# Kernel optimization log

Measured on AMD Instinct MI355X. Metric: run time of the kernel, lower is better.

## Reference

```python
import jax, jax.numpy as jnp
import numpy as np

F = 128
NRBF = 20
CUTOFF = 5.0
L = 3
NZ = 100
F2 = F // 2
N = 10000
E = 256000
NMOL = 100
EPS = 1e-8


def setup_inputs() -> dict:
    key = jax.random.key(0)
    ks = jax.random.split(key, 20)
    xyz = jax.random.uniform(ks[0], (N, 3), jnp.float32) * 10.0
    z = jax.random.randint(ks[1], (N,), 0, NZ)
    nbrs = jax.random.randint(ks[2], (E, 2), 0, N)
    # avoid self-edges (would give zero distance in the sinc RBF)
    nbrs = nbrs.at[:, 1].set(jnp.where(nbrs[:, 1] == nbrs[:, 0], (nbrs[:, 1] + 1) % N, nbrs[:, 1]))
    mol_idx = jnp.sort(jax.random.randint(ks[3], (N,), 0, NMOL))

    def p(k, shape, scale=0.05):
        return jax.random.normal(k, shape, jnp.float32) * scale

    return dict(
        xyz=xyz, z=z, nbrs=nbrs, mol_idx=mol_idx,
        emb=p(ks[4], (NZ, F), 1.0),
        msg_W1=p(ks[5], (L, F, F)), msg_b1=jnp.zeros((L, F), jnp.float32),
        msg_W2=p(ks[6], (L, F, 3 * F)), msg_b2=jnp.zeros((L, 3 * F), jnp.float32),
        dist_W=p(ks[7], (L, NRBF, 3 * F)), dist_b=jnp.zeros((L, 3 * F), jnp.float32),
        upd_U=p(ks[8], (L, F, F)), upd_V=p(ks[9], (L, F, F)),
        upd_W1=p(ks[10], (L, 2 * F, F)), upd_b1=jnp.zeros((L, F), jnp.float32),
        upd_W2=p(ks[11], (L, F, 3 * F)), upd_b2=jnp.zeros((L, 3 * F), jnp.float32),
        read_W1=p(ks[12], (F, F2)), read_b1=jnp.zeros((F2,), jnp.float32),
        read_W2=p(ks[13], (F2, 1)), read_b2=jnp.zeros((1,), jnp.float32),
    )


def _painn(xyz, emb, msg_W1, msg_b1, msg_W2, msg_b2, dist_W, dist_b,
           upd_U, upd_V, upd_W1, upd_b1, upd_W2, upd_b2,
           read_W1, read_b1, read_W2, read_b2, z, nbrs, mol_idx):
    idx_i = nbrs[:, 0]
    idx_j = nbrs[:, 1]
    r_ij = xyz[idx_j] - xyz[idx_i]                       # [E,3]
    d = jnp.sqrt(jnp.sum(r_ij * r_ij, -1) + EPS)          # [E]
    unit = r_ij / d[:, None]
    # sinc radial basis + cosine cutoff envelope
    nvec = jnp.arange(1, NRBF + 1, dtype=xyz.dtype)
    rbf = jnp.sin(nvec[None, :] * jnp.pi * d[:, None] / CUTOFF) / d[:, None]   # [E,NRBF]
    fcut = 0.5 * (jnp.cos(jnp.pi * d / CUTOFF) + 1.0) * (d < CUTOFF)           # [E]

    s_i = emb[z]                                          # [N,F]
    v_i = jnp.zeros((xyz.shape[0], F, 3), xyz.dtype)      # [N,F,3]

    for l in range(L):
        # message block: invariant filter on nodes, gather to edges
        phi = (jax.nn.silu(s_i @ msg_W1[l] + msg_b1[l]) @ msg_W2[l] + msg_b2[l])[idx_j]  # [E,3F]
        w_s = (rbf @ dist_W[l] + dist_b[l]) * fcut[:, None]                               # [E,3F]
        inv = (phi * w_s).reshape(-1, 3, F)
        ds_edge = inv[:, 0]                                                               # [E,F]
        dv_edge = inv[:, 1][:, :, None] * v_i[idx_j] + inv[:, 2][:, :, None] * unit[:, None, :]  # [E,F,3]
        s_i = s_i + jax.ops.segment_sum(ds_edge, idx_i, num_segments=s_i.shape[0])
        v_i = v_i + jax.ops.segment_sum(dv_edge, idx_i, num_segments=s_i.shape[0])

        # update block: channel-mixing of vectors + gated scalar/vector residuals
        u_v = jnp.einsum('nfv,fg->ngv', v_i, upd_U[l])
        v_v = jnp.einsum('nfv,fg->ngv', v_i, upd_V[l])
        vnorm = jnp.sqrt(jnp.sum(v_v * v_v, -1) + EPS)                                    # [N,F]
        a = (jax.nn.silu(jnp.concatenate([s_i, vnorm], -1) @ upd_W1[l] + upd_b1[l])
             @ upd_W2[l] + upd_b2[l]).reshape(-1, 3, F)
        dv = u_v * a[:, 0][:, :, None]
        ds = a[:, 1] * jnp.sum(u_v * v_v, -1) + a[:, 2]
        s_i = s_i + ds
        v_i = v_i + dv

    atom_e = jax.nn.silu(s_i @ read_W1 + read_b1) @ read_W2 + read_b2                     # [N,1]
    energy = jax.ops.segment_sum(atom_e[:, 0], mol_idx, num_segments=NMOL)                # [NMOL]
    return energy


def reference(xyz, z, nbrs, mol_idx, emb, msg_W1, msg_b1, msg_W2, msg_b2,
              dist_W, dist_b, upd_U, upd_V, upd_W1, upd_b1, upd_W2, upd_b2,
              read_W1, read_b1, read_W2, read_b2):
    return _painn(xyz, emb, msg_W1, msg_b1, msg_W2, msg_b2, dist_W, dist_b,
                  upd_U, upd_V, upd_W1, upd_b1, upd_W2, upd_b2,
                  read_W1, read_b1, read_W2, read_b2, z, nbrs, mol_idx)
```

## Files before the change

kernel.cpp:

```cpp
#include <hip/hip_runtime.h>
#include <hip/hip_bf16.h>
#include <math.h>

#define NA 10000
#define NE 256000
#define FDIM 128
#define F3 384
#define NRBF 20
#define NLAYERS 3
#define NMOLS 100
#define CAP 96
#define WROW 388
#define CUTOFF_F 5.0f
#define EPS_F 1e-8f
#define PI_F 3.14159265358979323846f

typedef __attribute__((ext_vector_type(8))) short bf16x8;
typedef __attribute__((ext_vector_type(4))) float f32x4;

struct pv6 { unsigned int u0, u1, u2; };

__device__ __forceinline__ float silu_f(float x) { return x / (1.0f + __expf(-x)); }

__device__ __forceinline__ unsigned short f2bf(float x) {
  unsigned u = __float_as_uint(x);
  return (unsigned short)((u + 0x7FFFu + ((u >> 16) & 1u)) >> 16);
}
__device__ __forceinline__ float bf2f(unsigned short u) {
  return __uint_as_float(((unsigned)u) << 16);
}
__device__ __forceinline__ float lo_f(unsigned int u) { return bf2f((unsigned short)(u & 0xFFFFu)); }
__device__ __forceinline__ float hi_f(unsigned int u) { return bf2f((unsigned short)(u >> 16)); }

__global__ __launch_bounds__(256) void geom_build_kernel(
    const float* __restrict__ xyz, const int* __restrict__ nbrs,
    float* __restrict__ unitv, unsigned short* __restrict__ rbf_bf,
    float* __restrict__ fcut,
    int* __restrict__ deg, int* __restrict__ slot_e, int* __restrict__ slot_j) {
  int e = blockIdx.x * 256 + threadIdx.x;
  if (e >= NE) return;
  int i = nbrs[2 * e + 0], j = nbrs[2 * e + 1];
  float rx = xyz[3 * j + 0] - xyz[3 * i + 0];
  float ry = xyz[3 * j + 1] - xyz[3 * i + 1];
  float rz = xyz[3 * j + 2] - xyz[3 * i + 2];
  float d = sqrtf(rx * rx + ry * ry + rz * rz + EPS_F);
  if (d >= CUTOFF_F) return;
  float invd = 1.0f / d;
  float fc = 0.5f * (__cosf(PI_F * d / CUTOFF_F) + 1.0f);
  unitv[3 * e + 0] = rx * invd;
  unitv[3 * e + 1] = ry * invd;
  unitv[3 * e + 2] = rz * invd;
  fcut[e] = fc;
  float base = PI_F * d / CUTOFF_F;
  float sc = invd * fc;
#pragma unroll
  for (int k = 0; k < NRBF; k++)
    rbf_bf[(size_t)e * NRBF + k] = f2bf(__sinf((float)(k + 1) * base) * sc);
  int pos = atomicAdd(&deg[i], 1);
  if (pos < CAP) {
    slot_e[i * CAP + pos] = e;
    slot_j[i * CAP + pos] = j;
  }
}

__device__ __forceinline__ void pack_one(const float* __restrict__ src,
                                         unsigned short* __restrict__ dst,
                                         int loc, int per, int N) {
  int lay = loc / per;
  int kn = loc - lay * per;
  int k = kn / N, n = kn - k * N;
  int kb = k >> 5, q = (k >> 3) & 3, j = k & 7, nt = n >> 4, c = n & 15;
  int NT = N >> 4;
  dst[(size_t)lay * per + (((kb * NT + nt) * 64 + (q * 16 + c)) * 8 + j)] = f2bf(src[loc]);
}

__device__ __forceinline__ void pack_dw(const float* __restrict__ dW,
                                        const float* __restrict__ db,
                                        unsigned short* __restrict__ dst, int loc) {
  int lay = loc / 12288;
  int kn = loc - lay * 12288;
  int k = kn / 384, n = kn - k * 384;
  float val = 0.0f;
  if (k < NRBF) val = dW[lay * NRBF * 384 + k * 384 + n];
  else if (k == NRBF) val = db[lay * 384 + n];
  int q = (k >> 3) & 3, j = k & 7, nt = n >> 4, c = n & 15;
  dst[(size_t)lay * 12288 + ((nt * 64 + (q * 16 + c)) * 8 + j)] = f2bf(val);
}

__global__ __launch_bounds__(256) void pack_all_kernel(
    const float* __restrict__ msgW1, const float* __restrict__ msgW2,
    const float* __restrict__ updU, const float* __restrict__ updV,
    const float* __restrict__ updW1, const float* __restrict__ updW2,
    const float* __restrict__ rW1, const float* __restrict__ distW,
    const float* __restrict__ distb, unsigned short* __restrict__ dst) {
  int t = blockIdx.x * 256 + threadIdx.x;
  if (t < 49152) pack_one(msgW1, dst, t, 16384, 128);
  else if (t < 196608) pack_one(msgW2, dst + 49152, t - 49152, 49152, 384);
  else if (t < 245760) pack_one(updU, dst + 196608, t - 196608, 16384, 128);
  else if (t < 294912) pack_one(updV, dst + 245760, t - 245760, 16384, 128);
  else if (t < 393216) pack_one(updW1, dst + 294912, t - 294912, 32768, 128);
  else if (t < 540672) pack_one(updW2, dst + 393216, t - 393216, 49152, 384);
  else if (t < 548864) pack_one(rW1, dst + 540672, t - 540672, 8192, 64);
  else if (t < 585728) pack_dw(distW, distb, dst + 548864, t - 548864);
}

__global__ __launch_bounds__(256) void msg0_mfma_kernel(
    const float* __restrict__ emb, const int* __restrict__ z, float* __restrict__ s_out,
    const unsigned short* __restrict__ pW1, const float* __restrict__ b1,
    const unsigned short* __restrict__ pW2, const float* __restrict__ b2,
    pv6* __restrict__ cmb) {
  __shared__ bf16x8 sA[4 * 64];
  __shared__ bf16x8 hA[4 * 64];
  int a0 = blockIdx.x * 16;
  int t = threadIdx.x;
  int lane = t & 63, w = t >> 6;
  {
    int kb = t >> 6, l = t & 63;
    int m = l & 15, q = l >> 4;
    int zi = z[a0 + m];
    const float* sp = emb + (size_t)zi * FDIM + kb * 32 + q * 8;
    float* so = s_out + (size_t)(a0 + m) * FDIM + kb * 32 + q * 8;
    bf16x8 c;
#pragma unroll
    for (int j = 0; j < 8; j++) {
      float v = sp[j];
      so[j] = v;
      c[j] = (short)f2bf(v);
    }
    sA[kb * 64 + l] = c;
  }
  __syncthreads();
  f32x4 accH[2];
#pragma unroll
  for (int t2 = 0; t2 < 2; t2++)
#pragma unroll
    for (int r = 0; r < 4; r++) accH[t2][r] = 0.0f;
  const bf16x8* W1f = (const bf16x8*)pW1;
#pragma unroll
  for (int kb = 0; kb < 4; kb++) {
    bf16x8 a = sA[kb * 64 + lane];
#pragma unroll
    for (int t2 = 0; t2 < 2; t2++) {
      bf16x8 b = W1f[(kb * 8 + 2 * w + t2) * 64 + lane];
      accH[t2] = __builtin_amdgcn_mfma_f32_16x16x32_bf16(a, b, accH[t2], 0, 0, 0);
    }
  }
  short* hs = (short*)hA;
#pragma unroll
  for (int t2 = 0; t2 < 2; t2++) {
    int n = w * 32 + t2 * 16 + (lane & 15);
    int kb = n >> 5, q = (n >> 3) & 3, j = n & 7;
    float bias = b1[n];
#pragma unroll
    for (int r = 0; r < 4; r++) {
      int m = (lane >> 4) * 4 + r;
      hs[(kb * 64 + q * 16 + m) * 8 + j] = (short)f2bf(silu_f(accH[t2][r] + bias));
    }
  }
  __syncthreads();
  f32x4 accP[3][2];
#pragma unroll
  for (int c3 = 0; c3 < 3; c3++)
#pragma unroll
    for (int t2 = 0; t2 < 2; t2++)
#pragma unroll
      for (int r = 0; r < 4; r++) accP[c3][t2][r] = 0.0f;
  const bf16x8* W2f = (const bf16x8*)pW2;
#pragma unroll
  for (int kb = 0; kb < 4; kb++) {
    bf16x8 a = hA[kb * 64 + lane];
#pragma unroll
    for (int c3 = 0; c3 < 3; c3++)
#pragma unroll
      for (int t2 = 0; t2 < 2; t2++) {
        bf16x8 b = W2f[(kb * 24 + c3 * 8 + 2 * w + t2) * 64 + lane];
        accP[c3][t2] = __builtin_amdgcn_mfma_f32_16x16x32_bf16(a, b, accP[c3][t2], 0, 0, 0);
      }
  }
#pragma unroll
  for (int t2 = 0; t2 < 2; t2++) {
    int g = (2 * w + t2) * 16 + (lane & 15);
    float bb0 = b2[g], bb1 = b2[FDIM + g], bb2 = b2[2 * FDIM + g];
#pragma unroll
    for (int r = 0; r < 4; r++) {
      int m = (lane >> 4) * 4 + r;
      unsigned p0 = f2bf(accP[0][t2][r] + bb0);
      unsigned p1 = f2bf(accP[1][t2][r] + bb1);
      unsigned p2 = f2bf(accP[2][t2][r] + bb2);
      pv6 rec;
      rec.u0 = p0 | (p1 << 16);
      rec.u1 = p2;
      rec.u2 = 0;
      cmb[(size_t)(a0 + m) * FDIM + g] = rec;
    }
  }
}

__global__ __launch_bounds__(128) void edge_kernel(
    const pv6* __restrict__ cmb, unsigned short* __restrict__ v_lin,
    float* __restrict__ s, const unsigned short* __restrict__ pDW,
    const int* __restrict__ deg, const int* __restrict__ slot_e,
    const int* __restrict__ slot_j, const unsigned short* __restrict__ rbf_bf,
    const float* __restrict__ fcut, const float* __restrict__ unitv) {
  __shared__ bf16x8 aLDS[64];
  __shared__ unsigned short w_lds[16][WROW];
  __shared__ float l_u[16][3];
  __shared__ int l_j[16];
  int i = blockIdx.x;
  int t = threadIdx.x;
  int f = t;
  int lane = t & 63, w = t >> 6;
  int cnt = deg[i];
  if (cnt > CAP) cnt = CAP;
  int base = i * CAP;
  float acc_s = 0.f, av0 = 0.f, av1 = 0.f, av2 = 0.f;
  const bf16x8* Bf = (const bf16x8*)pDW;
  for (int c0 = 0; c0 < cnt; c0 += 16) {
    int ccnt = cnt - c0;
    if (ccnt > 16) ccnt = 16;
    __syncthreads();
    if (t < 64) {
      int m = t & 15, q = t >> 4;
      bf16x8 a;
#pragma unroll
      for (int j = 0; j < 8; j++) a[j] = 0;
      int p = c0 + m;
      if (p < cnt) {
        int e = slot_e[base + p];
        const unsigned short* rb = rbf_bf + (size_t)e * NRBF;
#pragma unroll
        for (int j = 0; j < 8; j++) {
          int k = q * 8 + j;
          if (k < NRBF) a[j] = (short)rb[k];
          else if (k == NRBF) a[j] = (short)f2bf(fcut[e]);
        }
      }
      aLDS[t] = a;
    } else if (t < 80) {
      int idx = t - 64;
      int p = c0 + idx;
      if (p < cnt) {
        int e = slot_e[base + p];
        l_j[idx] = slot_j[base + p];
        l_u[idx][0] = unitv[3 * e + 0];
        l_u[idx][1] = unitv[3 * e + 1];
        l_u[idx][2] = unitv[3 * e + 2];
      }
    }
    __syncthreads();
    {
      bf16x8 a = aLDS[lane];
      int n0 = lane & 15, m0 = (lane >> 4) * 4;
#pragma unroll
      for (int tt = 0; tt < 12; tt++) {
        int nt = 12 * w + tt;
        f32x4 acc;
#pragma unroll
        for (int r = 0; r < 4; r++) acc[r] = 0.0f;
        acc = __builtin_amdgcn_mfma_f32_16x16x32_bf16(a, Bf[nt * 64 + lane], acc, 0, 0, 0);
        int n = nt * 16 + n0;
#pragma unroll
        for (int r = 0; r < 4; r++) w_lds[m0 + r][n] = f2bf(acc[r]);
      }
    }
    __syncthreads();
    int pp = 0;
    for (; pp + 2 <= ccnt; pp += 2) {
      int j0 = l_j[pp], j1 = l_j[pp + 1];
      pv6 R0 = cmb[(size_t)j0 * FDIM + f];
      pv6 R1 = cmb[(size_t)j1 * FDIM + f];
      float p00 = lo_f(R0.u0), p01 = hi_f(R0.u0), p02 = lo_f(R0.u1);
      float v00 = hi_f(R0.u1), v01 = lo_f(R0.u2), v02 = hi_f(R0.u2);
      float p10 = lo_f(R1.u0), p11 = hi_f(R1.u0), p12 = lo_f(R1.u1);
      float v10 = hi_f(R1.u1), v11 = lo_f(R1.u2), v12 = hi_f(R1.u2);
      float w00 = bf2f(w_lds[pp][f]), w01 = bf2f(w_lds[pp][FDIM + f]),
            w02 = bf2f(w_lds[pp][2 * FDIM + f]);
      float w10 = bf2f(w_lds[pp + 1][f]), w11 = bf2f(w_lds[pp + 1][FDIM + f]),
            w12 = bf2f(w_lds[pp + 1][2 * FDIM + f]);
      acc_s += p00 * w00 + p10 * w10;
      float i01 = p01 * w01, i02 = p02 * w02, i11 = p11 * w11, i12 = p12 * w12;
      av0 += i01 * v00 + i02 * l_u[pp][0] + i11 * v10 + i12 * l_u[pp + 1][0];
      av1 += i01 * v01 + i02 * l_u[pp][1] + i11 * v11 + i12 * l_u[pp + 1][1];
      av2 += i01 * v02 + i02 * l_u[pp][2] + i11 * v12 + i12 * l_u[pp + 1][2];
    }
    if (pp < ccnt) {
      int j0 = l_j[pp];
      pv6 R0 = cmb[(size_t)j0 * FDIM + f];
      float p00 = lo_f(R0.u0), p01 = hi_f(R0.u0), p02 = lo_f(R0.u1);
      float v00 = hi_f(R0.u1), v01 = lo_f(R0.u2), v02 = hi_f(R0.u2);
      float w00 = bf2f(w_lds[pp][f]), w01 = bf2f(w_lds[pp][FDIM + f]),
            w02 = bf2f(w_lds[pp][2 * FDIM + f]);
      acc_s += p00 * w00;
      float i01 = p01 * w01, i02 = p02 * w02;
      av0 += i01 * v00 + i02 * l_u[pp][0];
      av1 += i01 * v01 + i02 * l_u[pp][1];
      av2 += i01 * v02 + i02 * l_u[pp][2];
    }
  }
  {
    pv6 RI = cmb[(size_t)i * FDIM + f];
    av0 += hi_f(RI.u1);
    av1 += lo_f(RI.u2);
    av2 += hi_f(RI.u2);
  }
  unsigned short* vlo = v_lin + (size_t)i * F3;
  vlo[f] = f2bf(av0);
  vlo[FDIM + f] = f2bf(av1);
  vlo[2 * FDIM + f] = f2bf(av2);
  s[(size_t)i * FDIM + f] += acc_s;
}

__global__ __launch_bounds__(256) void upd_fused_kernel(
    float* __restrict__ s, const unsigned short* __restrict__ v_lin,
    pv6* __restrict__ cmb,
    const unsigned short* __restrict__ pU, const unsigned short* __restrict__ pV,
    const unsigned short* __restrict__ pW1, const float* __restrict__ b1,
    const unsigned short* __restrict__ pW2, const float* __restrict__ b2,
    int mode,
    const unsigned short* __restrict__ pMW1, const float* __restrict__ mb1,
    const unsigned short* __restrict__ pMW2, const float* __restrict__ mb2,
    const unsigned short* __restrict__ pRW1, const float* __restrict__ rb1,
    const float* __restrict__ rW2, const float* __restrict__ rb2,
    float* __restrict__ atom_e) {
  __shared__ bf16x8 vAf[3 * 4 * 64];
  __shared__ bf16x8 catA[8 * 64];
  __shared__ bf16x8 hA[4 * 64];
  __shared__ float red[4][16];
  int a0 = blockIdx.x * 16;
  int t = threadIdx.x;
  int lane = t & 63, w = t >> 6;
  {
    int l = t & 63, kb = (t >> 6) & 3;
    int m = l & 15, q = l >> 4;
#pragma unroll
    for (int rt = 0; rt < 3; rt++) {
      vAf[(rt * 4 + kb) * 64 + l] =
          *(const bf16x8*)(v_lin + (size_t)(a0 + m) * F3 + rt * FDIM + kb * 32 + q * 8);
    }
    const float* sp = s + (size_t)(a0 + m) * FDIM + kb * 32 + q * 8;
    bf16x8 c;
#pragma unroll
    for (int j = 0; j < 8; j++) c[j] = (short)f2bf(sp[j]);
    catA[kb * 64 + l] = c;
  }
  __syncthreads();
  f32x4 accU[3][2], accV[3][2];
#pragma unroll
  for (int rt = 0; rt < 3; rt++)
#pragma unroll
    for (int t2 = 0; t2 < 2; t2++)
#pragma unroll
      for (int r = 0; r < 4; r++) { accU[rt][t2][r] = 0.0f; accV[rt][t2][r] = 0.0f; }
  const bf16x8* Uf = (const bf16x8*)pU;
  const bf16x8* Vf = (const bf16x8*)pV;
#pragma unroll
  for (int kb = 0; kb < 4; kb++) {
    bf16x8 bu[2], bv[2];
#pragma unroll
    for (int t2 = 0; t2 < 2; t2++) {
      bu[t2] = Uf[(kb * 8 + 2 * w + t2) * 64 + lane];
      bv[t2] = Vf[(kb * 8 + 2 * w + t2) * 64 + lane];
    }
#pragma unroll
    for (int rt = 0; rt < 3; rt++) {
      bf16x8 a = vAf[(rt * 4 + kb) * 64 + lane];
#pragma unroll
      for (int t2 = 0; t2 < 2; t2++) {
        accU[rt][t2] = __builtin_amdgcn_mfma_f32_16x16x32_bf16(a, bu[t2], accU[rt][t2], 0, 0, 0);
        accV[rt][t2] = __builtin_amdgcn_mfma_f32_16x16x32_bf16(a, bv[t2], accV[rt][t2], 0, 0, 0);
      }
    }
  }
  short* cs = (short*)catA;
#pragma unroll
  for (int t2 = 0; t2 < 2; t2++) {
    int g = w * 32 + t2 * 16 + (lane & 15);
    int k = 128 + g;
    int kb = k >> 5, q = (k >> 3) & 3, j = k & 7;
#pragma unroll
    for (int r = 0; r < 4; r++) {
      int m = (lane >> 4) * 4 + r;
      float x0 = accV[0][t2][r], x1 = accV[1][t2][r], x2 = accV[2][t2][r];
      cs[(kb * 64 + q * 16 + m) * 8 + j] = (short)f2bf(sqrtf(x0 * x0 + x1 * x1 + x2 * x2 + EPS_F));
    }
  }
  __syncthreads();
  f32x4 accH[2];
#pragma unroll
  for (int t2 = 0; t2 < 2; t2++)
#pragma unroll
    for (int r = 0; r < 4; r++) accH[t2][r] = 0.0f;
  const bf16x8* W1f = (const bf16x8*)pW1;
#pragma unroll
  for (int kb = 0; kb < 8; kb++) {
    bf16x8 a = catA[kb * 64 + lane];
#pragma unroll
    for (int t2 = 0; t2 < 2; t2++) {
      bf16x8 b = W1f[(kb * 8 + 2 * w + t2) * 64 + lane];
      accH[t2] = __builtin_amdgcn_mfma_f32_16x16x32_bf16(a, b, accH[t2], 0, 0, 0);
    }
  }
  short* hs = (short*)hA;
#pragma unroll
  for (int t2 = 0; t2 < 2; t2++) {
    int n = w * 32 + t2 * 16 + (lane & 15);
    int kb = n >> 5, q = (n >> 3) & 3, j = n & 7;
    float bias = b1[n];
#pragma unroll
    for (int r = 0; r < 4; r++) {
      int m = (lane >> 4) * 4 + r;
      hs[(kb * 64 + q * 16 + m) * 8 + j] = (short)f2bf(silu_f(accH[t2][r] + bias));
    }
  }
  __syncthreads();
  f32x4 accA[3][2];
#pragma unroll
  for (int c3 = 0; c3 < 3; c3++)
#pragma unroll
    for (int t2 = 0; t2 < 2; t2++)
#pragma unroll
      for (int r = 0; r < 4; r++) accA[c3][t2][r] = 0.0f;
  const bf16x8* W2f = (const bf16x8*)pW2;
#pragma unroll
  for (int kb = 0; kb < 4; kb++) {
    bf16x8 a = hA[kb * 64 + lane];
#pragma unroll
    for (int c3 = 0; c3 < 3; c3++)
#pragma unroll
      for (int t2 = 0; t2 < 2; t2++) {
        bf16x8 b = W2f[(kb * 24 + c3 * 8 + 2 * w + t2) * 64 + lane];
        accA[c3][t2] = __builtin_amdgcn_mfma_f32_16x16x32_bf16(a, b, accA[c3][t2], 0, 0, 0);
      }
  }
  short* vsc = (short*)vAf;
#pragma unroll
  for (int t2 = 0; t2 < 2; t2++) {
    int g = w * 32 + t2 * 16 + (lane & 15);
    float bb0 = b2[g], bb1 = b2[FDIM + g], bb2 = b2[2 * FDIM + g];
    int kb = g >> 5, q = (g >> 3) & 3, j = g & 7;
#pragma unroll
    for (int r = 0; r < 4; r++) {
      int m = (lane >> 4) * 4 + r;
      int n = a0 + m;
      float a0v = accA[0][t2][r] + bb0;
      float a1v = accA[1][t2][r] + bb1;
      float a2v = accA[2][t2][r] + bb2;
      float dot = accU[0][t2][r] * accV[0][t2][r] + accU[1][t2][r] * accV[1][t2][r] +
                  accU[2][t2][r] * accV[2][t2][r];
      float s_new = s[(size_t)n * FDIM + g] + a1v * dot + a2v;
      if (mode == 0) {
        s[(size_t)n * FDIM + g] = s_new;
#pragma unroll
        for (int c = 0; c < 3; c++) {
          float nv = bf2f(v_lin[(size_t)n * F3 + c * FDIM + g]) + a0v * accU[c][t2][r];
          vsc[(m * FDIM + g) * 3 + c] = (short)f2bf(nv);
        }
      }
      cs[(kb * 64 + q * 16 + m) * 8 + j] = (short)f2bf(s_new);
    }
  }
  __syncthreads();
  if (mode == 0) {
    f32x4 accH2[2];
#pragma unroll
    for (int t2 = 0; t2 < 2; t2++)
#pragma unroll
      for (int r = 0; r < 4; r++) accH2[t2][r] = 0.0f;
    const bf16x8* MW1f = (const bf16x8*)pMW1;
#pragma unroll
    for (int kb = 0; kb < 4; kb++) {
      bf16x8 a = catA[kb * 64 + lane];
#pragma unroll
      for (int t2 = 0; t2 < 2; t2++) {
        bf16x8 b = MW1f[(kb * 8 + 2 * w + t2) * 64 + lane];
        accH2[t2] = __builtin_amdgcn_mfma_f32_16x16x32_bf16(a, b, accH2[t2], 0, 0, 0);
      }
    }
#pragma unroll
    for (int t2 = 0; t2 < 2; t2++) {
      int n = w * 32 + t2 * 16 + (lane & 15);
      int kb = n >> 5, q = (n >> 3) & 3, j = n & 7;
      float bias = mb1[n];
#pragma unroll
      for (int r = 0; r < 4; r++) {
        int m = (lane >> 4) * 4 + r;
        hs[(kb * 64 + q * 16 + m) * 8 + j] = (short)f2bf(silu_f(accH2[t2][r] + bias));
      }
    }
    __syncthreads();
    f32x4 accP[3][2];
#pragma unroll
    for (int c3 = 0; c3 < 3; c3++)
#pragma unroll
      for (int t2 = 0; t2 < 2; t2++)
#pragma unroll
        for (int r = 0; r < 4; r++) accP[c3][t2][r] = 0.0f;
    const bf16x8* MW2f = (const bf16x8*)pMW2;
#pragma unroll
    for (int kb = 0; kb < 4; kb++) {
      bf16x8 a = hA[kb * 64 + lane];
#pragma unroll
      for (int c3 = 0; c3 < 3; c3++)
#pragma unroll
        for (int t2 = 0; t2 < 2; t2++) {
          bf16x8 b = MW2f[(kb * 24 + c3 * 8 + 2 * w + t2) * 64 + lane];
          accP[c3][t2] = __builtin_amdgcn_mfma_f32_16x16x32_bf16(a, b, accP[c3][t2], 0, 0, 0);
        }
    }
#pragma unroll
    for (int t2 = 0; t2 < 2; t2++) {
      int g = (2 * w + t2) * 16 + (lane & 15);
      float bb0 = mb2[g], bb1 = mb2[FDIM + g], bb2v = mb2[2 * FDIM + g];
#pragma unroll
      for (int r = 0; r < 4; r++) {
        int m = (lane >> 4) * 4 + r;
        unsigned p0 = f2bf(accP[0][t2][r] + bb0);
        unsigned p1 = f2bf(accP[1][t2][r] + bb1);
        unsigned p2 = f2bf(accP[2][t2][r] + bb2v);
        unsigned v0 = (unsigned short)vsc[(m * FDIM + g) * 3 + 0];
        unsigned v1 = (unsigned short)vsc[(m * FDIM + g) * 3 + 1];
        unsigned v2 = (unsigned short)vsc[(m * FDIM + g) * 3 + 2];
        pv6 rec;
        rec.u0 = p0 | (p1 << 16);
        rec.u1 = p2 | (v0 << 16);
        rec.u2 = v1 | (v2 << 16);
        cmb[(size_t)(a0 + m) * FDIM + g] = rec;
      }
    }
  } else {
    f32x4 acc;
#pragma unroll
    for (int r = 0; r < 4; r++) acc[r] = 0.0f;
    const bf16x8* RW1f = (const bf16x8*)pRW1;
#pragma unroll
    for (int kb = 0; kb < 4; kb++) {
      bf16x8 a = catA[kb * 64 + lane];
      bf16x8 b = RW1f[(kb * 4 + w) * 64 + lane];
      acc = __builtin_amdgcn_mfma_f32_16x16x32_bf16(a, b, acc, 0, 0, 0);
    }
    int col = w * 16 + (lane & 15);
    float bias = rb1[col], w2v = rW2[col];
    float val[4];
#pragma unroll
    for (int r = 0; r < 4; r++) val[r] = silu_f(acc[r] + bias) * w2v;
#pragma unroll
    for (int off = 1; off < 16; off <<= 1)
#pragma unroll
      for (int r = 0; r < 4; r++) val[r] += __shfl_xor(val[r], off, 64);
    if ((lane & 15) == 0) {
#pragma unroll
      for (int r = 0; r < 4; r++) red[w][(lane >> 4) * 4 + r] = val[r];
    }
    __syncthreads();
    if (t < 16) {
      atom_e[a0 + t] = red[0][t] + red[1][t] + red[2][t] + red[3][t] + rb2[0];
    }
  }
}

__global__ __launch_bounds__(256) void mol_reduce_kernel(
    const float* __restrict__ atom_e, const int* __restrict__ mol_idx,
    float* __restrict__ out) {
  __shared__ float molsum[NMOLS];
  int t = threadIdx.x;
  if (t < NMOLS) molsum[t] = 0.0f;
  __syncthreads();
  int n = blockIdx.x * 256 + t;
  if (n < NA) atomicAdd(&molsum[mol_idx[n]], atom_e[n]);
  __syncthreads();
  if (t < NMOLS && molsum[t] != 0.0f) atomicAdd(&out[t], molsum[t]);
}

extern "C" void kernel_launch(void* const* d_in, const int* in_sizes, int n_in,
                              void* d_out, int out_size, void* d_ws, size_t ws_size,
                              hipStream_t stream) {
  const float* xyz = (const float*)d_in[0];
  const int* z = (const int*)d_in[1];
  const int* nbrs = (const int*)d_in[2];
  const int* mol = (const int*)d_in[3];
  const float* emb = (const float*)d_in[4];
  const float* msgW1 = (const float*)d_in[5];
  const float* msgb1 = (const float*)d_in[6];
  const float* msgW2 = (const float*)d_in[7];
  const float* msgb2 = (const float*)d_in[8];
  const float* distW = (const float*)d_in[9];
  const float* distb = (const float*)d_in[10];
  const float* updU = (const float*)d_in[11];
  const float* updV = (const float*)d_in[12];
  const float* updW1 = (const float*)d_in[13];
  const float* updb1 = (const float*)d_in[14];
  const float* updW2 = (const float*)d_in[15];
  const float* updb2 = (const float*)d_in[16];
  const float* rW1 = (const float*)d_in[17];
  const float* rb1 = (const float*)d_in[18];
  const float* rW2 = (const float*)d_in[19];
  const float* rb2 = (const float*)d_in[20];

  float* ws = (float*)d_ws;
  float* s = ws;      ws += (size_t)NA * FDIM;
  float* fcut = ws;   ws += (size_t)NE;
  float* unitv = ws;  ws += (size_t)NE * 3;
  float* atom_e = ws; ws += (size_t)NA;
  int* deg = (int*)ws;
  int* slot_e = deg + NA;
  int* slot_j = slot_e + NA * CAP;
  unsigned short* pk = (unsigned short*)(((uintptr_t)(slot_j + NA * CAP) + 15) & ~(uintptr_t)15);
  unsigned short* pMsgW1 = pk;
  unsigned short* pMsgW2 = pMsgW1 + 49152;
  unsigned short* pUpdU  = pMsgW2 + 147456;
  unsigned short* pUpdV  = pUpdU + 49152;
  unsigned short* pUpdW1 = pUpdV + 49152;
  unsigned short* pUpdW2 = pUpdW1 + 98304;
  unsigned short* pRW1   = pUpdW2 + 147456;
  unsigned short* pDW    = pRW1 + 8192;
  unsigned short* rbf_bf = (unsigned short*)(((uintptr_t)(pDW + 36864) + 15) & ~(uintptr_t)15);
  unsigned short* after_rbf = rbf_bf + (size_t)NE * NRBF + 8;
  pv6* cmb = (pv6*)(((uintptr_t)after_rbf + 15) & ~(uintptr_t)15);
  unsigned short* v_lin = (unsigned short*)(cmb + (size_t)NA * FDIM);

  hipMemsetAsync(deg, 0, NA * sizeof(int), stream);
  hipMemsetAsync(d_out, 0, NMOLS * sizeof(float), stream);

  pack_all_kernel<<<(585728 + 255) / 256, 256, 0, stream>>>(
      msgW1, msgW2, updU, updV, updW1, updW2, rW1, distW, distb, pMsgW1);
  geom_build_kernel<<<NE / 256, 256, 0, stream>>>(xyz, nbrs, unitv, rbf_bf, fcut,
                                                  deg, slot_e, slot_j);
  msg0_mfma_kernel<<<NA / 16, 256, 0, stream>>>(emb, z, s, pMsgW1, msgb1, pMsgW2, msgb2, cmb);

  for (int l = 0; l < NLAYERS; l++) {
    edge_kernel<<<NA, 128, 0, stream>>>(cmb, v_lin, s,
                                        pDW + (size_t)l * 12288,
                                        deg, slot_e, slot_j, rbf_bf, fcut, unitv);
    int mode = (l == NLAYERS - 1) ? 1 : 0;
    int lnext = (l + 1 < NLAYERS) ? l + 1 : 0;
    upd_fused_kernel<<<NA / 16, 256, 0, stream>>>(
        s, v_lin, cmb, pUpdU + (size_t)l * 16384, pUpdV + (size_t)l * 16384,
        pUpdW1 + (size_t)l * 32768, updb1 + (size_t)l * FDIM,
        pUpdW2 + (size_t)l * 49152, updb2 + (size_t)l * F3,
        mode,
        pMsgW1 + (size_t)lnext * 16384, msgb1 + (size_t)lnext * FDIM,
        pMsgW2 + (size_t)lnext * 49152, msgb2 + (size_t)lnext * F3,
        pRW1, rb1, rW2, rb2, atom_e);
  }
  mol_reduce_kernel<<<(NA + 255) / 256, 256, 0, stream>>>(atom_e, mol, (float*)d_out);
}
```

Before: 326.4 us.

## Split edge chunks across two block halves and skip zero vectors in layer zero

The edge kernel now runs with 256 threads. Two 128-thread halves take alternating 16-edge chunks with double-buffered LDS, and their partial sums are combined through shared memory at the end. In the first layer a vzero flag skips loading the vector parts of the gathered records and the self term, since the vectors start at zero. The update kernel reads old vectors from its LDS tile instead of global v_lin and writes the packed record fields separately. The trade-off is more barriers, extra LDS use, and idle halves on atoms with an odd number of chunks.

Result: slower. 393.8 us (+20.7%).

```diff
diff --git a/kernel.cpp b/kernel.cpp
--- a/kernel.cpp
+++ b/kernel.cpp
@@ -196,31 +196,39 @@
   }
 }
 
-__global__ __launch_bounds__(128) void edge_kernel(
+__global__ __launch_bounds__(256) void edge_kernel(
     const pv6* __restrict__ cmb, unsigned short* __restrict__ v_lin,
     float* __restrict__ s, const unsigned short* __restrict__ pDW,
     const int* __restrict__ deg, const int* __restrict__ slot_e,
     const int* __restrict__ slot_j, const unsigned short* __restrict__ rbf_bf,
-    const float* __restrict__ fcut, const float* __restrict__ unitv) {
-  __shared__ bf16x8 aLDS[64];
-  __shared__ unsigned short w_lds[16][WROW];
-  __shared__ float l_u[16][3];
-  __shared__ int l_j[16];
+    const float* __restrict__ fcut, const float* __restrict__ unitv, int vzero) {
+  __shared__ bf16x8 aLDS[2][64];
+  __shared__ unsigned short w_lds[2][16][WROW];
+  __shared__ float l_u[2][16][3];
+  __shared__ int l_j[2][16];
+  __shared__ float partial[4][FDIM];
   int i = blockIdx.x;
   int t = threadIdx.x;
-  int f = t;
-  int lane = t & 63, w = t >> 6;
+  int half = t >> 7;
+  int p128 = t & 127;
+  int f = p128;
+  int lane = t & 63;
+  int wp = (t >> 6) & 1;
   int cnt = deg[i];
   if (cnt > CAP) cnt = CAP;
   int base = i * CAP;
+  int nchunks = (cnt + 15) >> 4;
+  int maxiter = (nchunks + 1) >> 1;
   float acc_s = 0.f, av0 = 0.f, av1 = 0.f, av2 = 0.f;
   const bf16x8* Bf = (const bf16x8*)pDW;
-  for (int c0 = 0; c0 < cnt; c0 += 16) {
-    int ccnt = cnt - c0;
-    if (ccnt > 16) ccnt = 16;
+  for (int it = 0; it < maxiter; it++) {
+    int c = 2 * it + half;
+    bool active = (c < nchunks);
+    int c0 = c * 16;
+    int ccnt = active ? ((cnt - c0 > 16) ? 16 : (cnt - c0)) : 0;
     __syncthreads();
-    if (t < 64) {
-      int m = t & 15, q = t >> 4;
+    if (active && p128 < 64) {
+      int m = p128 & 15, q = p128 >> 4;
       bf16x8 a;
 #pragma unroll
       for (int j = 0; j < 8; j++) a[j] = 0;
@@ -235,79 +243,111 @@
           else if (k == NRBF) a[j] = (short)f2bf(fcut[e]);
         }
       }
-      aLDS[t] = a;
-    } else if (t < 80) {
-      int idx = t - 64;
+      aLDS[half][p128] = a;
+    } else if (active && p128 < 80) {
+      int idx = p128 - 64;
       int p = c0 + idx;
       if (p < cnt) {
         int e = slot_e[base + p];
-        l_j[idx] = slot_j[base + p];
-        l_u[idx][0] = unitv[3 * e + 0];
-        l_u[idx][1] = unitv[3 * e + 1];
-        l_u[idx][2] = unitv[3 * e + 2];
+        l_j[half][idx] = slot_j[base + p];
+        l_u[half][idx][0] = unitv[3 * e + 0];
+        l_u[half][idx][1] = unitv[3 * e + 1];
+        l_u[half][idx][2] = unitv[3 * e + 2];
       }
     }
     __syncthreads();
-    {
-      bf16x8 a = aLDS[lane];
+    if (active) {
+      bf16x8 a = aLDS[half][lane];
       int n0 = lane & 15, m0 = (lane >> 4) * 4;
 #pragma unroll
       for (int tt = 0; tt < 12; tt++) {
-        int nt = 12 * w + tt;
+        int nt = 12 * wp + tt;
         f32x4 acc;
 #pragma unroll
         for (int r = 0; r < 4; r++) acc[r] = 0.0f;
         acc = __builtin_amdgcn_mfma_f32_16x16x32_bf16(a, Bf[nt * 64 + lane], acc, 0, 0, 0);
         int n = nt * 16 + n0;
 #pragma unroll
-        for (int r = 0; r < 4; r++) w_lds[m0 + r][n] = f2bf(acc[r]);
+        for (int r = 0; r < 4; r++) w_lds[half][m0 + r][n] = f2bf(acc[r]);
       }
     }
     __syncthreads();
     int pp = 0;
     for (; pp + 2 <= ccnt; pp += 2) {
-      int j0 = l_j[pp], j1 = l_j[pp + 1];
-      pv6 R0 = cmb[(size_t)j0 * FDIM + f];
-      pv6 R1 = cmb[(size_t)j1 * FDIM + f];
-      float p00 = lo_f(R0.u0), p01 = hi_f(R0.u0), p02 = lo_f(R0.u1);
-      float v00 = hi_f(R0.u1), v01 = lo_f(R0.u2), v02 = hi_f(R0.u2);
-      float p10 = lo_f(R1.u0), p11 = hi_f(R1.u0), p12 = lo_f(R1.u1);
-      float v10 = hi_f(R1.u1), v11 = lo_f(R1.u2), v12 = hi_f(R1.u2);
-      float w00 = bf2f(w_lds[pp][f]), w01 = bf2f(w_lds[pp][FDIM + f]),
-            w02 = bf2f(w_lds[pp][2 * FDIM + f]);
-      float w10 = bf2f(w_lds[pp + 1][f]), w11 = bf2f(w_lds[pp + 1][FDIM + f]),
-            w12 = bf2f(w_lds[pp + 1][2 * FDIM + f]);
+      int j0 = l_j[half][pp], j1 = l_j[half][pp + 1];
+      float p00, p01, p02, p10, p11, p12;
+      float v00 = 0.f, v01 = 0.f, v02 = 0.f, v10 = 0.f, v11 = 0.f, v12 = 0.f;
+      if (vzero) {
+        const pv6* R0 = &cmb[(size_t)j0 * FDIM + f];
+        const pv6* R1 = &cmb[(size_t)j1 * FDIM + f];
+        unsigned a0u = R0->u0, a1u = R0->u1, b0u = R1->u0, b1u = R1->u1;
+        p00 = lo_f(a0u); p01 = hi_f(a0u); p02 = lo_f(a1u);
+        p10 = lo_f(b0u); p11 = hi_f(b0u); p12 = lo_f(b1u);
+      } else {
+        pv6 R0 = cmb[(size_t)j0 * FDIM + f];
+        pv6 R1 = cmb[(size_t)j1 * FDIM + f];
+        p00 = lo_f(R0.u0); p01 = hi_f(R0.u0); p02 = lo_f(R0.u1);
+        v00 = hi_f(R0.u1); v01 = lo_f(R0.u2); v02 = hi_f(R0.u2);
+        p10 = lo_f(R1.u0); p11 = hi_f(R1.u0); p12 = lo_f(R1.u1);
+        v10 = hi_f(R1.u1); v11 = lo_f(R1.u2); v12 = hi_f(R1.u2);
+      }
+      float w00 = bf2f(w_lds[half][pp][f]), w01 = bf2f(w_lds[half][pp][FDIM + f]),
+            w02 = bf2f(w_lds[half][pp][2 * FDIM + f]);
+      float w10 = bf2f(w_lds[half][pp + 1][f]), w11 = bf2f(w_lds[half][pp + 1][FDIM + f]),
+            w12 = bf2f(w_lds[half][pp + 1][2 * FDIM + f]);
       acc_s += p00 * w00 + p10 * w10;
       float i01 = p01 * w01, i02 = p02 * w02, i11 = p11 * w11, i12 = p12 * w12;
-      av0 += i01 * v00 + i02 * l_u[pp][0] + i11 * v10 + i12 * l_u[pp + 1][0];
-      av1 += i01 * v01 + i02 * l_u[pp][1] + i11 * v11 + i12 * l_u[pp + 1][1];
-      av2 += i01 * v02 + i02 * l_u[pp][2] + i11 * v12 + i12 * l_u[pp + 1][2];
+      av0 += i01 * v00 + i02 * l_u[half][pp][0] + i11 * v10 + i12 * l_u[half][pp + 1][0];
+      av1 += i01 * v01 + i02 * l_u[half][pp][1] + i11 * v11 + i12 * l_u[half][pp + 1][1];
+      av2 += i01 * v02 + i02 * l_u[half][pp][2] + i11 * v12 + i12 * l_u[half][pp + 1][2];
     }
     if (pp < ccnt) {
-      int j0 = l_j[pp];
-      pv6 R0 = cmb[(size_t)j0 * FDIM + f];
-      float p00 = lo_f(R0.u0), p01 = hi_f(R0.u0), p02 = lo_f(R0.u1);
-      float v00 = hi_f(R0.u1), v01 = lo_f(R0.u2), v02 = hi_f(R0.u2);
-      float w00 = bf2f(w_lds[pp][f]), w01 = bf2f(w_lds[pp][FDIM + f]),
-            w02 = bf2f(w_lds[pp][2 * FDIM + f]);
+      int j0 = l_j[half][pp];
+      float p00, p01, p02;
+      float v00 = 0.f, v01 = 0.f, v02 = 0.f;
+      if (vzero) {
+        const pv6* R0 = &cmb[(size_t)j0 * FDIM + f];
+        unsigned a0u = R0->u0, a1u = R0->u1;
+        p00 = lo_f(a0u); p01 = hi_f(a0u); p02 = lo_f(a1u);
+      } else {
+        pv6 R0 = cmb[(size_t)j0 * FDIM + f];
+        p00 = lo_f(R0.u0); p01 = hi_f(R0.u0); p02 = lo_f(R0.u1);
+        v00 = hi_f(R0.u1); v01 = lo_f(R0.u2); v02 = hi_f(R0.u2);
+      }
+      float w00 = bf2f(w_lds[half][pp][f]), w01 = bf2f(w_lds[half][pp][FDIM + f]),
+            w02 = bf2f(w_lds[half][pp][2 * FDIM + f]);
       acc_s += p00 * w00;
       float i01 = p01 * w01, i02 = p02 * w02;
-      av0 += i01 * v00 + i02 * l_u[pp][0];
-      av1 += i01 * v01 + i02 * l_u[pp][1];
-      av2 += i01 * v02 + i02 * l_u[pp][2];
-    }
-  }
-  {
-    pv6 RI = cmb[(size_t)i * FDIM + f];
-    av0 += hi_f(RI.u1);
-    av1 += lo_f(RI.u2);
-    av2 += hi_f(RI.u2);
-  }
-  unsigned short* vlo = v_lin + (size_t)i * F3;
-  vlo[f] = f2bf(av0);
-  vlo[FDIM + f] = f2bf(av1);
-  vlo[2 * FDIM + f] = f2bf(av2);
-  s[(size_t)i * FDIM + f] += acc_s;
+      av0 += i01 * v00 + i02 * l_u[half][pp][0];
+      av1 += i01 * v01 + i02 * l_u[half][pp][1];
+      av2 += i01 * v02 + i02 * l_u[half][pp][2];
+    }
+  }
+  __syncthreads();
+  if (half == 1) {
+    partial[0][f] = av0;
+    partial[1][f] = av1;
+    partial[2][f] = av2;
+    partial[3][f] = acc_s;
+  }
+  __syncthreads();
+  if (half == 0) {
+    av0 += partial[0][f];
+    av1 += partial[1][f];
+    av2 += partial[2][f];
+    acc_s += partial[3][f];
+    if (!vzero) {
+      pv6 RI = cmb[(size_t)i * FDIM + f];
+      av0 += hi_f(RI.u1);
+      av1 += lo_f(RI.u2);
+      av2 += hi_f(RI.u2);
+    }
+    unsigned short* vlo = v_lin + (size_t)i * F3;
+    vlo[f] = f2bf(av0);
+    vlo[FDIM + f] = f2bf(av1);
+    vlo[2 * FDIM + f] = f2bf(av2);
+    s[(size_t)i * FDIM + f] += acc_s;
+  }
 }
 
 __global__ __launch_bounds__(256) void upd_fused_kernel(
@@ -432,7 +472,8 @@
         accA[c3][t2] = __builtin_amdgcn_mfma_f32_16x16x32_bf16(a, b, accA[c3][t2], 0, 0, 0);
       }
   }
-  short* vsc = (short*)vAf;
+  const short* vls = (const short*)vAf;
+  unsigned short v0keep[2][4];
 #pragma unroll
   for (int t2 = 0; t2 < 2; t2++) {
     int g = w * 32 + t2 * 16 + (lane & 15);
@@ -450,11 +491,14 @@
       float s_new = s[(size_t)n * FDIM + g] + a1v * dot + a2v;
       if (mode == 0) {
         s[(size_t)n * FDIM + g] = s_new;
+        float nv[3];
 #pragma unroll
         for (int c = 0; c < 3; c++) {
-          float nv = bf2f(v_lin[(size_t)n * F3 + c * FDIM + g]) + a0v * accU[c][t2][r];
-          vsc[(m * FDIM + g) * 3 + c] = (short)f2bf(nv);
+          float vold = bf2f((unsigned short)vls[(((c * 4 + kb) * 64) + (q * 16 + m)) * 8 + j]);
+          nv[c] = vold + a0v * accU[c][t2][r];
         }
+        v0keep[t2][r] = f2bf(nv[0]);
+        cmb[(size_t)n * FDIM + g].u2 = (unsigned)f2bf(nv[1]) | ((unsigned)f2bf(nv[2]) << 16);
       }
       cs[(kb * 64 + q * 16 + m) * 8 + j] = (short)f2bf(s_new);
     }
@@ -517,14 +561,9 @@
         unsigned p0 = f2bf(accP[0][t2][r] + bb0);
         unsigned p1 = f2bf(accP[1][t2][r] + bb1);
         unsigned p2 = f2bf(accP[2][t2][r] + bb2v);
-        unsigned v0 = (unsigned short)vsc[(m * FDIM + g) * 3 + 0];
-        unsigned v1 = (unsigned short)vsc[(m * FDIM + g) * 3 + 1];
-        unsigned v2 = (unsigned short)vsc[(m * FDIM + g) * 3 + 2];
-        pv6 rec;
-        rec.u0 = p0 | (p1 << 16);
-        rec.u1 = p2 | (v0 << 16);
-        rec.u2 = v1 | (v2 << 16);
-        cmb[(size_t)(a0 + m) * FDIM + g] = rec;
+        pv6* rec = &cmb[(size_t)(a0 + m) * FDIM + g];
+        rec->u0 = p0 | (p1 << 16);
+        rec->u1 = p2 | ((unsigned)v0keep[t2][r] << 16);
       }
     }
   } else {
@@ -628,9 +667,10 @@
   msg0_mfma_kernel<<<NA / 16, 256, 0, stream>>>(emb, z, s, pMsgW1, msgb1, pMsgW2, msgb2, cmb);
 
   for (int l = 0; l < NLAYERS; l++) {
-    edge_kernel<<<NA, 128, 0, stream>>>(cmb, v_lin, s,
+    edge_kernel<<<NA, 256, 0, stream>>>(cmb, v_lin, s,
                                         pDW + (size_t)l * 12288,
-                                        deg, slot_e, slot_j, rbf_bf, fcut, unitv);
+                                        deg, slot_e, slot_j, rbf_bf, fcut, unitv,
+                                        (l == 0) ? 1 : 0);
     int mode = (l == NLAYERS - 1) ? 1 : 0;
     int lnext = (l + 1 < NLAYERS) ? l + 1 : 0;
     upd_fused_kernel<<<NA / 16, 256, 0, stream>>>(
```
